# Optimization experiments

Hardware: AMD Instinct MI355X
Metric: run time of the kernel (lower is better)

## Reference

```python
import jax, jax.numpy as jnp
import numpy as np

HIDDEN = 2048
NUM_HEADS = 16
NUM_KV_HEADS = 4
HEAD_DIM = HIDDEN // NUM_HEADS  # 128
GROUPS = NUM_HEADS // NUM_KV_HEADS  # 4
ROPE_DIMS = 32
QK_GAIN = 6.0
B, T = 2, 2048


def _rope_cos_sin(T, dtype):
    pos = jnp.arange(T, dtype=jnp.float32)
    inv_freq = 1.0 / (10000.0 ** (jnp.arange(0, ROPE_DIMS, 2, dtype=jnp.float32) / ROPE_DIMS))
    freqs = jnp.outer(pos, inv_freq)                  # [T, ROPE/2]
    freqs = jnp.concatenate([freqs, freqs], axis=-1)  # [T, ROPE]
    return jnp.cos(freqs).astype(dtype), jnp.sin(freqs).astype(dtype)


def _apply_rope(t, cos_f, sin_f):
    # t: [B, H, T, head_dim]; rope on first ROPE_DIMS, pass-through on the rest
    t_rt, t_pass = t[..., :ROPE_DIMS], t[..., ROPE_DIMS:]
    h1, h2 = jnp.split(t_rt, 2, axis=-1)
    rot = jnp.concatenate([-h2, h1], axis=-1)
    return jnp.concatenate([t_rt * cos_f + rot * sin_f, t_pass], axis=-1)


def setup_inputs() -> dict:
    key = jax.random.key(0)
    ks = jax.random.split(key, 5)
    s = 0.02
    return {
        "x": jax.random.normal(ks[0], (B, T, HIDDEN), jnp.float32),
        "Wq": jax.random.normal(ks[1], (HIDDEN, HIDDEN), jnp.float32) * s,
        "Wk": jax.random.normal(ks[2], (HIDDEN, NUM_KV_HEADS * HEAD_DIM), jnp.float32) * s,
        "Wv": jax.random.normal(ks[3], (HIDDEN, NUM_KV_HEADS * HEAD_DIM), jnp.float32) * s,
        "Wo": jax.random.normal(ks[4], (HIDDEN, HIDDEN), jnp.float32) * s,
    }


def reference(x, Wq, Wk, Wv, Wo):
    Bx, Tx, C = x.shape
    q = (x @ Wq).reshape(Bx, Tx, NUM_HEADS, HEAD_DIM).transpose(0, 2, 1, 3)      # [B,H,T,d]
    k = (x @ Wk).reshape(Bx, Tx, NUM_KV_HEADS, HEAD_DIM).transpose(0, 2, 1, 3)   # [B,KV,T,d]
    v = (x @ Wv).reshape(Bx, Tx, NUM_KV_HEADS, HEAD_DIM).transpose(0, 2, 1, 3)   # [B,KV,T,d]

    cos_f, sin_f = _rope_cos_sin(Tx, q.dtype)  # [T, ROPE]
    q = _apply_rope(q, cos_f, sin_f)
    k = _apply_rope(k, cos_f, sin_f)

    # GQA: group query heads per kv head instead of repeat_interleave-ing K/V
    qg = q.reshape(Bx, NUM_KV_HEADS, GROUPS, Tx, HEAD_DIM)
    scale = QK_GAIN / jnp.sqrt(jnp.asarray(HEAD_DIM, q.dtype))
    scores = jnp.einsum('bkgqd,bkld->bkgql', qg * scale, k)  # [B,KV,G,T,T]
    causal = jnp.tril(jnp.ones((Tx, Tx), dtype=bool))
    scores = jnp.where(causal, scores, jnp.asarray(-jnp.inf, scores.dtype))
    probs = jax.nn.softmax(scores, axis=-1)
    out = jnp.einsum('bkgql,bkld->bkgqd', probs, v)          # [B,KV,G,T,d]
    out = out.reshape(Bx, NUM_HEADS, Tx, HEAD_DIM).transpose(0, 2, 1, 3).reshape(Bx, Tx, C)
    return out @ Wo
```

## Files before the change

### kernel.cpp

```cpp
#include <hip/hip_runtime.h>
#include <hip/hip_bf16.h>
#include <cstdint>
#include <cstddef>

typedef unsigned short u16;
typedef short s16x8 __attribute__((ext_vector_type(8)));
typedef float f32x4 __attribute__((ext_vector_type(4)));
typedef float f32x16 __attribute__((ext_vector_type(16)));
typedef u16 u16x4 __attribute__((ext_vector_type(4)));

#define HIDDEN_C 2048
#define TSEQ 2048
#define BATCH 2
#define NHEADS 16
#define NKV 4
#define HDIM 128
#define NQKV 3072
#define BTR 4096
#define QK_SCALE 0.53033008588991f

__device__ __forceinline__ float bf2f(u16 u) {
  union { uint32_t i; float f; } v; v.i = ((uint32_t)u) << 16; return v.f;
}
__device__ __forceinline__ u16 f2bf(float f) {
  union { float f; uint32_t i; } v; v.f = f;
  uint32_t r = v.i + 0x7fffu + ((v.i >> 16) & 1u);
  return (u16)(r >> 16);
}

#define AS1(p) ((__attribute__((address_space(1))) void*)(uintptr_t)(p))
#define AS3(p) ((__attribute__((address_space(3))) void*)(p))

__global__ void prep_kernel(const float* __restrict__ x, u16* __restrict__ xb,
                            float2* __restrict__ tab,
                            const float* __restrict__ Wq,
                            const float* __restrict__ Wk,
                            const float* __restrict__ Wv,
                            const float* __restrict__ Wo,
                            u16* __restrict__ wqkvT,
                            u16* __restrict__ woT) {
  const int z = blockIdx.z;
  int tx = threadIdx.x, ty = threadIdx.y;
  if (z == 4) {
    int tid = ty * 32 + tx;
    int bid = blockIdx.y * 64 + blockIdx.x;
    int gi = bid * 256 + tid;
    if (gi < TSEQ * 16) {
      int t = gi >> 4, i = gi & 15;
      float f = powf(10000.f, -(float)i * (1.f / 16.f));
      float ang = (float)t * f;
      tab[gi] = make_float2(cosf(ang), sinf(ang));
    }
    int i = gi * 8;
    float4 a = *(const float4*)(x + i);
    float4 b = *(const float4*)(x + i + 4);
    uint4 o;
    o.x = (uint32_t)f2bf(a.x) | ((uint32_t)f2bf(a.y) << 16);
    o.y = (uint32_t)f2bf(a.z) | ((uint32_t)f2bf(a.w) << 16);
    o.z = (uint32_t)f2bf(b.x) | ((uint32_t)f2bf(b.y) << 16);
    o.w = (uint32_t)f2bf(b.z) | ((uint32_t)f2bf(b.w) << 16);
    *(uint4*)(xb + i) = o;
    return;
  }
  const float* in; u16* out; int C;
  switch (z) {
    case 0: in = Wq; out = wqkvT;                        C = 2048; break;
    case 1: in = Wk; out = wqkvT + (size_t)2048 * 2048;  C = 512;  break;
    case 2: in = Wv; out = wqkvT + (size_t)2560 * 2048;  C = 512;  break;
    default: in = Wo; out = woT;                         C = 2048; break;
  }
  int r0 = blockIdx.y * 32, c0 = blockIdx.x * 32;
  if (c0 >= C) return;
  __shared__ float tile[32][33];
  #pragma unroll
  for (int i = 0; i < 32; i += 8)
    tile[ty + i][tx] = in[(size_t)(r0 + ty + i) * C + c0 + tx];
  __syncthreads();
  #pragma unroll
  for (int i = 0; i < 32; i += 8)
    out[(size_t)(c0 + ty + i) * 2048 + r0 + tx] = f2bf(tile[tx][ty + i]);
}

template <typename OutT>
__global__ __launch_bounds__(256) void gemm_bt_kernel(const u16* __restrict__ A,
                                                      const u16* __restrict__ BT,
                                                      OutT* __restrict__ C,
                                                      int M, int N, int K,
                                                      const float2* __restrict__ tab,
                                                      int mode) {
  __shared__ u16 As[128 * 64];
  __shared__ u16 Bs[128 * 64];
  const int tid = threadIdx.x;
  const int wave = tid >> 6, lane = tid & 63;
  const int lr = lane & 15, lg = lane >> 4;
  const int m0 = blockIdx.y * 128, n0 = blockIdx.x * 128;
  const int wr = wave >> 1, wc = wave & 1;
  const int fsw = (lr & 7) << 3;
  f32x4 acc[4][4];
  #pragma unroll
  for (int a = 0; a < 4; ++a)
    #pragma unroll
    for (int b = 0; b < 4; ++b) acc[a][b] = (f32x4){0.f, 0.f, 0.f, 0.f};

  for (int k0 = 0; k0 < K; k0 += 64) {
    #pragma unroll
    for (int i = 0; i < 4; ++i) {
      int c = tid + i * 256;
      int row = c >> 3, slot = c & 7;
      int gslot = slot ^ (row & 7);
      const u16* gA = A + (size_t)(m0 + row) * K + k0 + gslot * 8;
      const u16* gB = BT + (size_t)(n0 + row) * K + k0 + gslot * 8;
      char* lA = (char*)As + (size_t)c * 16;
      char* lB = (char*)Bs + (size_t)c * 16;
      __builtin_amdgcn_global_load_lds(AS1(gA), AS3(lA), 16, 0, 0);
      __builtin_amdgcn_global_load_lds(AS1(gB), AS3(lB), 16, 0, 0);
    }
    __syncthreads();
    #pragma unroll
    for (int kk = 0; kk < 2; ++kk) {
      s16x8 af[4], bfr[4];
      #pragma unroll
      for (int mi = 0; mi < 4; ++mi)
        af[mi] = *(const s16x8*)(As + (wr * 64 + mi * 16 + lr) * 64 + ((kk * 32 + lg * 8) ^ fsw));
      #pragma unroll
      for (int ni = 0; ni < 4; ++ni)
        bfr[ni] = *(const s16x8*)(Bs + (wc * 64 + ni * 16 + lr) * 64 + ((kk * 32 + lg * 8) ^ fsw));
      #pragma unroll
      for (int mi = 0; mi < 4; ++mi)
        #pragma unroll
        for (int ni = 0; ni < 4; ++ni)
          acc[mi][ni] = __builtin_amdgcn_mfma_f32_16x16x32_bf16(af[mi], bfr[ni], acc[mi][ni], 0, 0, 0);
    }
    __syncthreads();
  }
  if (mode) {
    if (n0 < 2560 && wc == 0) {
      #pragma unroll
      for (int mi = 0; mi < 4; ++mi) {
        int rowb = m0 + wr * 64 + mi * 16 + lg * 4;
        #pragma unroll
        for (int r = 0; r < 4; ++r) {
          int t = (rowb + r) & (TSEQ - 1);
          float2 cs = tab[(t << 4) | lr];
          float a = acc[mi][0][r], b2 = acc[mi][1][r];
          acc[mi][0][r] = a * cs.x - b2 * cs.y;
          acc[mi][1][r] = b2 * cs.x + a * cs.y;
        }
      }
    }
    if (n0 < 2048) {
      #pragma unroll
      for (int mi = 0; mi < 4; ++mi)
        #pragma unroll
        for (int ni = 0; ni < 4; ++ni)
          #pragma unroll
          for (int r = 0; r < 4; ++r) acc[mi][ni][r] *= QK_SCALE;
    }
  }
  #pragma unroll
  for (int mi = 0; mi < 4; ++mi) {
    int rowb = m0 + wr * 64 + mi * 16 + lg * 4;
    #pragma unroll
    for (int ni = 0; ni < 4; ++ni) {
      int col = n0 + wc * 64 + ni * 16 + lr;
      #pragma unroll
      for (int r = 0; r < 4; ++r) {
        float v = acc[mi][ni][r];
        if constexpr (sizeof(OutT) == 2) C[(size_t)(rowb + r) * N + col] = (OutT)f2bf(v);
        else                             C[(size_t)(rowb + r) * N + col] = v;
      }
    }
  }
}

__global__ void transpose_v_kernel(const u16* __restrict__ qkv, u16* __restrict__ vt) {
  int bg = blockIdx.z;
  int b = bg >> 2, g = bg & 3;
  int t0 = blockIdx.x * 32, d0 = blockIdx.y * 32;
  __shared__ u16 tile[32][33];
  int tx = threadIdx.x, ty = threadIdx.y;
  #pragma unroll
  for (int i = 0; i < 32; i += 8)
    tile[ty + i][tx] = qkv[(size_t)(b * TSEQ + t0 + ty + i) * NQKV + 2560 + g * HDIM + d0 + tx];
  __syncthreads();
  #pragma unroll
  for (int i = 0; i < 32; i += 8)
    vt[((size_t)bg * HDIM + d0 + ty + i) * TSEQ + t0 + tx] = tile[tx][ty + i];
}

__global__ __launch_bounds__(256, 2) void attn_kernel(const u16* __restrict__ qkv,
                                                      const u16* __restrict__ vt,
                                                      u16* __restrict__ h0out,
                                                      u16* __restrict__ h1out,
                                                      float2* __restrict__ ml) {
  __shared__ u16 K_lds[2][64][128];
  __shared__ u16 V_lds[2][128][64];
  __shared__ u16 P_lds[4][32][64];

  const int idx = blockIdx.x;
  const int tile = 15 - (idx >> 6);
  const int half = idx & 1;
  const int bh = (idx >> 1) & 31;
  const int h = bh & 15, b = bh >> 4, g = h >> 2;
  const int tid = threadIdx.x, w = tid >> 6, lane = tid & 63;
  const int lq = lane & 31;
  const int hf = lane >> 5;
  const int q0 = tile * 128;
  const int q0w = q0 + w * 32;
  const int kswz = (lq & 15) << 3;
  const int vswz = (lane & 7) << 3;
  const int pswz = lq & 7;

  const u16* Qg = qkv + (size_t)b * TSEQ * NQKV + h * HDIM;
  const u16* Kg = qkv + (size_t)b * TSEQ * NQKV + HIDDEN_C + g * HDIM;
  const u16* Vg = vt + (size_t)(b * NKV + g) * HDIM * TSEQ;

  s16x8 aq[8];
  {
    const u16* qrow = Qg + (size_t)(q0w + lq) * NQKV + hf * 8;
    #pragma unroll
    for (int ds = 0; ds < 8; ++ds) aq[ds] = *(const s16x8*)(qrow + ds * 16);
  }

  f32x16 O[4];
  #pragma unroll
  for (int dt = 0; dt < 4; ++dt)
    #pragma unroll
    for (int r = 0; r < 16; ++r) O[dt][r] = 0.f;
  float m_r = -1e30f, l_r = 0.f;

  auto STAGE = [&](int buf, int kb) {
    #pragma unroll
    for (int i = 0; i < 4; ++i) {
      int c = tid + i * 256;
      int row = c >> 4, slot = c & 15;
      int gslot = slot ^ (row & 15);
      const u16* src = Kg + (size_t)(kb + row) * NQKV + gslot * 8;
      char* dst = (char*)&K_lds[buf][0][0] + (size_t)c * 16;
      __builtin_amdgcn_global_load_lds(AS1(src), AS3(dst), 16, 0, 0);
    }
    #pragma unroll
    for (int i = 0; i < 4; ++i) {
      int c = tid + i * 256;
      int row = c >> 3, slot = c & 7;
      int gslot = slot ^ (row & 7);
      const u16* src = Vg + (size_t)row * TSEQ + kb + gslot * 8;
      char* dst = (char*)&V_lds[buf][0][0] + (size_t)c * 16;
      __builtin_amdgcn_global_load_lds(AS1(src), AS3(dst), 16, 0, 0);
    }
  };

  const int t0i = half * (tile + 1);
  const int t1i = t0i + (tile + 1);
  STAGE(0, t0i * 64);
  asm volatile("s_waitcnt vmcnt(0)" ::: "memory");
  __syncthreads();

  for (int tt = t0i; tt < t1i; ++tt) {
    const int kb = tt * 64;
    const int cur = (tt - t0i) & 1;
    if (tt + 1 < t1i) STAGE(cur ^ 1, kb + 64);

    if (kb <= q0w + 31) {
      f32x16 S[2];
      #pragma unroll
      for (int kh = 0; kh < 2; ++kh)
        #pragma unroll
        for (int r = 0; r < 16; ++r) S[kh][r] = 0.f;
      __builtin_amdgcn_s_setprio(1);
      #pragma unroll
      for (int kh = 0; kh < 2; ++kh) {
        const u16* krow = &K_lds[cur][kh * 32 + lq][0];
        #pragma unroll
        for (int ds = 0; ds < 8; ++ds) {
          s16x8 ak = *(const s16x8*)(krow + ((ds * 16 + hf * 8) ^ kswz));
          S[kh] = __builtin_amdgcn_mfma_f32_32x32x16_bf16(ak, aq[ds], S[kh], 0, 0, 0);
        }
      }
      __builtin_amdgcn_s_setprio(0);
      if (kb + 63 > q0w) {
        const int q = q0w + lq;
        #pragma unroll
        for (int kh = 0; kh < 2; ++kh)
          #pragma unroll
          for (int r = 0; r < 16; ++r) {
            int k = kb + kh * 32 + (r & 3) + 8 * (r >> 2) + 4 * hf;
            if (k > q) S[kh][r] = -1e30f;
          }
      }
      f32x16 pm;
      #pragma unroll
      for (int r = 0; r < 16; ++r) pm[r] = fmaxf(S[0][r], S[1][r]);
      float m8[8];
      #pragma unroll
      for (int r = 0; r < 8; ++r) m8[r] = fmaxf(pm[r], pm[r + 8]);
      float mx = fmaxf(fmaxf(fmaxf(m8[0], m8[4]), fmaxf(m8[1], m8[5])),
                       fmaxf(fmaxf(m8[2], m8[6]), fmaxf(m8[3], m8[7])));
      mx = fmaxf(mx, __shfl_xor(mx, 32));
      if (!__all(mx <= m_r + 8.f)) {
        const float mn = fmaxf(m_r, mx);
        const float al = __expf(m_r - mn);
        m_r = mn;
        l_r *= al;
        #pragma unroll
        for (int dt = 0; dt < 4; ++dt)
          #pragma unroll
          for (int r = 0; r < 16; ++r) O[dt][r] *= al;
      }
      #pragma unroll
      for (int kh = 0; kh < 2; ++kh)
        #pragma unroll
        for (int r = 0; r < 16; ++r) S[kh][r] = __expf(S[kh][r] - m_r);
      f32x16 sv;
      #pragma unroll
      for (int r = 0; r < 16; ++r) sv[r] = S[0][r] + S[1][r];
      float s8[8];
      #pragma unroll
      for (int r = 0; r < 8; ++r) s8[r] = sv[r] + sv[r + 8];
      float ps = ((s8[0] + s8[4]) + (s8[1] + s8[5])) + ((s8[2] + s8[6]) + (s8[3] + s8[7]));
      ps += __shfl_xor(ps, 32);
      l_r += ps;
      u16* pw = &P_lds[w][lq][0];
      #pragma unroll
      for (int kh = 0; kh < 2; ++kh)
        #pragma unroll
        for (int r2 = 0; r2 < 4; ++r2) {
          u16x4 hq;
          #pragma unroll
          for (int j = 0; j < 4; ++j) hq[j] = f2bf(S[kh][r2 * 4 + j]);
          int slot = kh * 4 + r2;
          *(u16x4*)(pw + ((slot ^ pswz) << 3) + hf * 4) = hq;
        }
      asm volatile("s_waitcnt lgkmcnt(0)" ::: "memory");
      __builtin_amdgcn_sched_barrier(0);
      s16x8 pb[4];
      #pragma unroll
      for (int ks = 0; ks < 4; ++ks) {
        int slot = ks * 2 + hf;
        pb[ks] = *(const s16x8*)(pw + ((slot ^ pswz) << 3));
      }
      __builtin_amdgcn_s_setprio(1);
      #pragma unroll
      for (int dt = 0; dt < 4; ++dt) {
        const u16* vrow = &V_lds[cur][dt * 32 + lq][0];
        #pragma unroll
        for (int ks = 0; ks < 4; ++ks) {
          s16x8 av = *(const s16x8*)(vrow + ((ks * 16 + hf * 8) ^ vswz));
          O[dt] = __builtin_amdgcn_mfma_f32_32x32x16_bf16(av, pb[ks], O[dt], 0, 0, 0);
        }
      }
      __builtin_amdgcn_s_setprio(0);
    }
    asm volatile("s_waitcnt vmcnt(0)" ::: "memory");
    __syncthreads();
  }

  const float invl = (l_r > 0.f) ? 1.f / l_r : 0.f;
  u16* obase = (half ? h1out : h0out);
  u16* orow = obase + (size_t)(b * TSEQ + q0w + lq) * HIDDEN_C + h * HDIM + hf * 4;
  #pragma unroll
  for (int dt = 0; dt < 4; ++dt)
    #pragma unroll
    for (int r2 = 0; r2 < 4; ++r2) {
      u16x4 o4;
      #pragma unroll
      for (int j = 0; j < 4; ++j) o4[j] = f2bf(O[dt][r2 * 4 + j] * invl);
      *(u16x4*)(orow + dt * 32 + r2 * 8) = o4;
    }
  if (hf == 0)
    ml[(((size_t)half * BATCH + b) * NHEADS + h) * TSEQ + q0w + lq] = make_float2(m_r, l_r);
}

__global__ void combine_kernel(const u16* __restrict__ h0, u16* __restrict__ h1out,
                               const float2* __restrict__ ml) {
  int gi = blockIdx.x * blockDim.x + threadIdx.x;
  size_t base = (size_t)gi * 8;
  int bt = (int)(base >> 11);
  int c = (int)(base & 2047);
  int h = c >> 7;
  int b = bt >> 11, q = bt & (TSEQ - 1);
  float2 v0 = ml[((size_t)(0 * BATCH + b) * NHEADS + h) * TSEQ + q];
  float2 v1 = ml[((size_t)(1 * BATCH + b) * NHEADS + h) * TSEQ + q];
  float m = fmaxf(v0.x, v1.x);
  float w0 = v0.y * __expf(v0.x - m);
  float w1 = v1.y * __expf(v1.x - m);
  float inv = 1.f / (w0 + w1);
  w0 *= inv; w1 *= inv;
  uint4 a = *(const uint4*)(h0 + base);
  uint4 d = *(const uint4*)(h1out + base);
  const uint32_t* au = (const uint32_t*)&a;
  const uint32_t* du = (const uint32_t*)&d;
  uint4 o;
  uint32_t* ou = (uint32_t*)&o;
  #pragma unroll
  for (int j = 0; j < 4; ++j) {
    float lo = bf2f((u16)(au[j] & 0xffff)) * w0 + bf2f((u16)(du[j] & 0xffff)) * w1;
    float hi = bf2f((u16)(au[j] >> 16)) * w0 + bf2f((u16)(du[j] >> 16)) * w1;
    ou[j] = (uint32_t)f2bf(lo) | ((uint32_t)f2bf(hi) << 16);
  }
  *(uint4*)(h1out + base) = o;
}

extern "C" void kernel_launch(void* const* d_in, const int* in_sizes, int n_in,
                              void* d_out, int out_size, void* d_ws, size_t ws_size,
                              hipStream_t stream) {
  const float* x  = (const float*)d_in[0];
  const float* Wq = (const float*)d_in[1];
  const float* Wk = (const float*)d_in[2];
  const float* Wv = (const float*)d_in[3];
  const float* Wo = (const float*)d_in[4];
  float* out = (float*)d_out;
  char* ws = (char*)d_ws;

  u16* xb    = (u16*)(ws);
  u16* wqkvT = (u16*)(ws + (size_t)(16u << 20));
  u16* woT   = (u16*)(ws + (size_t)(28u << 20));
  u16* qkv   = (u16*)(ws + (size_t)(36u << 20));
  u16* vtb   = (u16*)(ws + (size_t)(60u << 20));
  u16* attn  = (u16*)(ws + (size_t)(64u << 20));
  float2* rope_tab = (float2*)(ws + (size_t)(64u << 20));
  float2* mlbuf = (float2*)(ws + (size_t)(80u << 20));

  dim3 tb(32, 8);
  prep_kernel<<<dim3(64, 64, 5), tb, 0, stream>>>(x, xb, rope_tab, Wq, Wk, Wv, Wo, wqkvT, woT);

  gemm_bt_kernel<u16><<<dim3(NQKV / 128, BTR / 128), 256, 0, stream>>>(
      xb, wqkvT, qkv, BTR, NQKV, HIDDEN_C, rope_tab, 1);

  transpose_v_kernel<<<dim3(TSEQ / 32, HDIM / 32, BATCH * NKV), tb, 0, stream>>>(qkv, vtb);

  attn_kernel<<<1024, 256, 0, stream>>>(qkv, vtb, xb, attn, mlbuf);

  combine_kernel<<<(BTR * HIDDEN_C / 8) / 256, 256, 0, stream>>>(xb, attn, mlbuf);

  gemm_bt_kernel<float><<<dim3(HIDDEN_C / 128, BTR / 128), 256, 0, stream>>>(
      attn, woT, out, BTR, HIDDEN_C, HIDDEN_C, nullptr, 0);
}
```

Before: 206.7 us.

## Halve attention KV tile, raise occupancy, reorder tiles, swizzle GEMM block order

The attention kernel now processes 32-key blocks instead of 64, shrinking K/V/P shared-memory buffers and register state so launch bounds can request 4 blocks per CU. The causal query-tile order is interleaved across quarters of the grid to balance heavy and light tiles per dispatch wave. Separately, the GEMM remaps block indices with an 8-way swizzle to improve L2 locality. Smaller key tiles double loop iterations, barriers and softmax rescale overhead per unit of work.

Result: slower. 271.5 us (+31.4%).

```diff
diff --git a/kernel.cpp b/kernel.cpp
--- a/kernel.cpp
+++ b/kernel.cpp
@@ -93,7 +93,11 @@
   const int tid = threadIdx.x;
   const int wave = tid >> 6, lane = tid & 63;
   const int lr = lane & 15, lg = lane >> 4;
-  const int m0 = blockIdx.y * 128, n0 = blockIdx.x * 128;
+  const int gx = gridDim.x;
+  const int bid = blockIdx.y * gx + blockIdx.x;
+  const int cpx = (gx * gridDim.y) >> 3;
+  const int swzb = (bid & 7) * cpx + (bid >> 3);
+  const int m0 = (swzb / gx) * 128, n0 = (swzb % gx) * 128;
   const int wr = wave >> 1, wc = wave & 1;
   const int fsw = (lr & 7) << 3;
   f32x4 acc[4][4];
@@ -188,17 +192,19 @@
     vt[((size_t)bg * HDIM + d0 + ty + i) * TSEQ + t0 + tx] = tile[tx][ty + i];
 }
 
-__global__ __launch_bounds__(256, 2) void attn_kernel(const u16* __restrict__ qkv,
+__global__ __launch_bounds__(256, 4) void attn_kernel(const u16* __restrict__ qkv,
                                                       const u16* __restrict__ vt,
                                                       u16* __restrict__ h0out,
                                                       u16* __restrict__ h1out,
                                                       float2* __restrict__ ml) {
-  __shared__ u16 K_lds[2][64][128];
-  __shared__ u16 V_lds[2][128][64];
-  __shared__ u16 P_lds[4][32][64];
+  __shared__ u16 K_lds[2][32][128];
+  __shared__ u16 V_lds[2][128][32];
+  __shared__ u16 P_lds[4][32][32];
 
   const int idx = blockIdx.x;
-  const int tile = 15 - (idx >> 6);
+  const int slot4 = idx >> 6;
+  const int qd = slot4 >> 2, pp = slot4 & 3;
+  const int tile = (qd == 0) ? 15 - pp : (qd == 1) ? 8 + pp : (qd == 2) ? 7 - pp : pp;
   const int half = idx & 1;
   const int bh = (idx >> 1) & 31;
   const int h = bh & 15, b = bh >> 4, g = h >> 2;
@@ -208,8 +214,8 @@
   const int q0 = tile * 128;
   const int q0w = q0 + w * 32;
   const int kswz = (lq & 15) << 3;
-  const int vswz = (lane & 7) << 3;
-  const int pswz = lq & 7;
+  const int vswz = (lq & 3) << 3;
+  const int pswz = lq & 3;
 
   const u16* Qg = qkv + (size_t)b * TSEQ * NQKV + h * HDIM;
   const u16* Kg = qkv + (size_t)b * TSEQ * NQKV + HIDDEN_C + g * HDIM;
@@ -231,69 +237,61 @@
 
   auto STAGE = [&](int buf, int kb) {
     #pragma unroll
-    for (int i = 0; i < 4; ++i) {
+    for (int i = 0; i < 2; ++i) {
       int c = tid + i * 256;
-      int row = c >> 4, slot = c & 15;
-      int gslot = slot ^ (row & 15);
+      int row = c >> 4, sl = c & 15;
+      int gslot = sl ^ (row & 15);
       const u16* src = Kg + (size_t)(kb + row) * NQKV + gslot * 8;
       char* dst = (char*)&K_lds[buf][0][0] + (size_t)c * 16;
       __builtin_amdgcn_global_load_lds(AS1(src), AS3(dst), 16, 0, 0);
     }
     #pragma unroll
-    for (int i = 0; i < 4; ++i) {
+    for (int i = 0; i < 2; ++i) {
       int c = tid + i * 256;
-      int row = c >> 3, slot = c & 7;
-      int gslot = slot ^ (row & 7);
+      int row = c >> 2, sl = c & 3;
+      int gslot = sl ^ (row & 3);
       const u16* src = Vg + (size_t)row * TSEQ + kb + gslot * 8;
       char* dst = (char*)&V_lds[buf][0][0] + (size_t)c * 16;
       __builtin_amdgcn_global_load_lds(AS1(src), AS3(dst), 16, 0, 0);
     }
   };
 
-  const int t0i = half * (tile + 1);
-  const int t1i = t0i + (tile + 1);
-  STAGE(0, t0i * 64);
+  const int t0i = half * 2 * (tile + 1);
+  const int t1i = t0i + 2 * (tile + 1);
+  STAGE(0, t0i * 32);
   asm volatile("s_waitcnt vmcnt(0)" ::: "memory");
   __syncthreads();
 
   for (int tt = t0i; tt < t1i; ++tt) {
-    const int kb = tt * 64;
+    const int kb = tt * 32;
     const int cur = (tt - t0i) & 1;
-    if (tt + 1 < t1i) STAGE(cur ^ 1, kb + 64);
+    if (tt + 1 < t1i) STAGE(cur ^ 1, kb + 32);
 
     if (kb <= q0w + 31) {
-      f32x16 S[2];
-      #pragma unroll
-      for (int kh = 0; kh < 2; ++kh)
-        #pragma unroll
-        for (int r = 0; r < 16; ++r) S[kh][r] = 0.f;
+      f32x16 S;
+      #pragma unroll
+      for (int r = 0; r < 16; ++r) S[r] = 0.f;
       __builtin_amdgcn_s_setprio(1);
-      #pragma unroll
-      for (int kh = 0; kh < 2; ++kh) {
-        const u16* krow = &K_lds[cur][kh * 32 + lq][0];
+      {
+        const u16* krow = &K_lds[cur][lq][0];
         #pragma unroll
         for (int ds = 0; ds < 8; ++ds) {
           s16x8 ak = *(const s16x8*)(krow + ((ds * 16 + hf * 8) ^ kswz));
-          S[kh] = __builtin_amdgcn_mfma_f32_32x32x16_bf16(ak, aq[ds], S[kh], 0, 0, 0);
+          S = __builtin_amdgcn_mfma_f32_32x32x16_bf16(ak, aq[ds], S, 0, 0, 0);
         }
       }
       __builtin_amdgcn_s_setprio(0);
-      if (kb + 63 > q0w) {
+      if (kb + 31 > q0w) {
         const int q = q0w + lq;
         #pragma unroll
-        for (int kh = 0; kh < 2; ++kh)
-          #pragma unroll
-          for (int r = 0; r < 16; ++r) {
-            int k = kb + kh * 32 + (r & 3) + 8 * (r >> 2) + 4 * hf;
-            if (k > q) S[kh][r] = -1e30f;
-          }
-      }
-      f32x16 pm;
-      #pragma unroll
-      for (int r = 0; r < 16; ++r) pm[r] = fmaxf(S[0][r], S[1][r]);
+        for (int r = 0; r < 16; ++r) {
+          int k = kb + (r & 3) + 8 * (r >> 2) + 4 * hf;
+          if (k > q) S[r] = -1e30f;
+        }
+      }
       float m8[8];
       #pragma unroll
-      for (int r = 0; r < 8; ++r) m8[r] = fmaxf(pm[r], pm[r + 8]);
+      for (int r = 0; r < 8; ++r) m8[r] = fmaxf(S[r], S[r + 8]);
       float mx = fmaxf(fmaxf(fmaxf(m8[0], m8[4]), fmaxf(m8[1], m8[5])),
                        fmaxf(fmaxf(m8[2], m8[6]), fmaxf(m8[3], m8[7])));
       mx = fmaxf(mx, __shfl_xor(mx, 32));
@@ -308,43 +306,35 @@
           for (int r = 0; r < 16; ++r) O[dt][r] *= al;
       }
       #pragma unroll
-      for (int kh = 0; kh < 2; ++kh)
-        #pragma unroll
-        for (int r = 0; r < 16; ++r) S[kh][r] = __expf(S[kh][r] - m_r);
-      f32x16 sv;
-      #pragma unroll
-      for (int r = 0; r < 16; ++r) sv[r] = S[0][r] + S[1][r];
+      for (int r = 0; r < 16; ++r) S[r] = __expf(S[r] - m_r);
       float s8[8];
       #pragma unroll
-      for (int r = 0; r < 8; ++r) s8[r] = sv[r] + sv[r + 8];
+      for (int r = 0; r < 8; ++r) s8[r] = S[r] + S[r + 8];
       float ps = ((s8[0] + s8[4]) + (s8[1] + s8[5])) + ((s8[2] + s8[6]) + (s8[3] + s8[7]));
       ps += __shfl_xor(ps, 32);
       l_r += ps;
       u16* pw = &P_lds[w][lq][0];
       #pragma unroll
-      for (int kh = 0; kh < 2; ++kh)
-        #pragma unroll
-        for (int r2 = 0; r2 < 4; ++r2) {
-          u16x4 hq;
-          #pragma unroll
-          for (int j = 0; j < 4; ++j) hq[j] = f2bf(S[kh][r2 * 4 + j]);
-          int slot = kh * 4 + r2;
-          *(u16x4*)(pw + ((slot ^ pswz) << 3) + hf * 4) = hq;
-        }
+      for (int r2 = 0; r2 < 4; ++r2) {
+        u16x4 hq;
+        #pragma unroll
+        for (int j = 0; j < 4; ++j) hq[j] = f2bf(S[r2 * 4 + j]);
+        *(u16x4*)(pw + ((r2 ^ pswz) << 3) + hf * 4) = hq;
+      }
       asm volatile("s_waitcnt lgkmcnt(0)" ::: "memory");
       __builtin_amdgcn_sched_barrier(0);
-      s16x8 pb[4];
-      #pragma unroll
-      for (int ks = 0; ks < 4; ++ks) {
-        int slot = ks * 2 + hf;
-        pb[ks] = *(const s16x8*)(pw + ((slot ^ pswz) << 3));
+      s16x8 pb[2];
+      #pragma unroll
+      for (int ks = 0; ks < 2; ++ks) {
+        int psl = ks * 2 + hf;
+        pb[ks] = *(const s16x8*)(pw + ((psl ^ pswz) << 3));
       }
       __builtin_amdgcn_s_setprio(1);
       #pragma unroll
       for (int dt = 0; dt < 4; ++dt) {
         const u16* vrow = &V_lds[cur][dt * 32 + lq][0];
         #pragma unroll
-        for (int ks = 0; ks < 4; ++ks) {
+        for (int ks = 0; ks < 2; ++ks) {
           s16x8 av = *(const s16x8*)(vrow + ((ks * 16 + hf * 8) ^ vswz));
           O[dt] = __builtin_amdgcn_mfma_f32_32x32x16_bf16(av, pb[ks], O[dt], 0, 0, 0);
         }
```
